# Kernel tuning notes

Measured on AMD Instinct MI355X. Metric: run time of the kernel, lower is better.

## Reference

```python
import jax, jax.numpy as jnp
import numpy as np

G, B, N, D = 3, 4096, 32, 256
C, H, A, L = 128, 8, 128, 16


def setup_inputs() -> dict:
    key = jax.random.key(0)
    ks = jax.random.split(key, 9)
    return {
        "targets": jax.random.normal(ks[0], (B, D), jnp.float32),
        "contexts": jax.random.normal(ks[1], (G, B, N, D), jnp.float32),
        "kernel": jax.random.normal(ks[2], (D, C), jnp.float32) * 0.05,
        "attn_kernel": jax.random.normal(ks[3], (1, H, 2 * C), jnp.float32) * 0.05,
        "attn_bias": jnp.zeros((H * C,), jnp.float32),
        "sem_kernel": jax.random.normal(ks[4], (H * C, A), jnp.float32) * 0.05,
        "sem_att_kernel": jax.random.normal(ks[5], (A, 1), jnp.float32) * 0.05,
        "dense_w": jax.random.normal(ks[6], (H * C, L), jnp.float32) * 0.05,
        "dense_b": jnp.zeros((L,), jnp.float32),
    }


def reference(targets, contexts, kernel, attn_kernel, attn_bias, sem_kernel,
              sem_att_kernel, dense_w, dense_b):
    # NodeAttention (shared weights across metapath groups; vectorized over G)
    node = jnp.einsum('bd,dc->bc', targets, kernel)            # [B,C]
    neigh = jnp.einsum('gbnd,dc->gbnc', contexts, kernel)      # [G,B,N,C]
    g, b, n, c = neigh.shape
    ak = attn_kernel[0]                                        # [H,2C]
    ak_node, ak_neigh = ak[:, :c], ak[:, c:]                   # split of concat([node, neigh])
    # scores[g,b,n,h] = concat(node_b, neigh_gbn) . ak_h
    scores = (jnp.einsum('bc,hc->bh', node, ak_node)[None, :, None, :]
              + jnp.einsum('gbnc,hc->gbnh', neigh, ak_neigh))  # [G,B,N,H]
    scores = jnp.transpose(scores, (0, 1, 3, 2))               # [G,B,H,N]
    coef = jax.nn.softmax(jax.nn.leaky_relu(scores, 0.2), axis=-1)
    z = jnp.einsum('gbhn,gbnc->gbhc', coef, neigh)             # [G,B,H,C]
    z = z.reshape(g, b, -1) + attn_bias                        # [G,B,H*C] (concat=True)
    # SemanticAttention over metapath groups
    inp = jnp.transpose(z, (1, 0, 2))                          # [B,G,HC]
    s = jnp.squeeze(jnp.matmul(jnp.tanh(jnp.matmul(inp, sem_kernel)), sem_att_kernel), -1)  # [B,G]
    att = jax.nn.softmax(s, axis=-1)
    pooled = jnp.einsum('bg,bgd->bd', att, inp)                # [B,HC]
    logits = pooled @ dense_w + dense_b                        # [B,L]
    return logits
```

## Files before the change

### kernel.cpp

```cpp
#include <hip/hip_runtime.h>
#include <hip/hip_bf16.h>

typedef float v4f __attribute__((ext_vector_type(4)));
typedef short v8s __attribute__((ext_vector_type(8)));

__device__ __forceinline__ unsigned short f2bf(float x){
    unsigned u = __float_as_uint(x);
    u += 0x7FFFu + ((u >> 16) & 1u);
    return (unsigned short)(u >> 16);
}
__device__ __forceinline__ float bf2f(unsigned short h){
    return __uint_as_float(((unsigned)h) << 16);
}
__device__ __forceinline__ v8s pack_bf8(v4f a, v4f b){
    union { v8s s; __hip_bfloat162 h[4]; } u;
    u.h[0] = __float22bfloat162_rn(float2{a[0],a[1]});
    u.h[1] = __float22bfloat162_rn(float2{a[2],a[3]});
    u.h[2] = __float22bfloat162_rn(float2{b[0],b[1]});
    u.h[3] = __float22bfloat162_rn(float2{b[2],b[3]});
    return u.s;
}

__global__ __launch_bounds__(256) void prep_all(const float* __restrict__ targ,
        const float* __restrict__ kern, const float* __restrict__ ak,
        const float* __restrict__ semk, float* __restrict__ ns,
        unsigned short* __restrict__ packB, unsigned short* __restrict__ pack2){
    __shared__ float wsh[256*8];
    int blk = blockIdx.x, t = threadIdx.x;
    if (blk < 16){
        {
            float a[8];
            #pragma unroll
            for (int h=0;h<8;h++) a[h]=0.f;
            const float* kr = kern + t*128;
            for (int c=0;c<128;c++){
                float kv = kr[c];
                #pragma unroll
                for (int h=0;h<8;h++) a[h] = fmaf(kv, ak[h*256+c], a[h]);
            }
            #pragma unroll
            for (int h=0;h<8;h++) wsh[t*8+h]=a[h];
        }
        __syncthreads();
        int b = blk*256 + t;
        float acc[8];
        #pragma unroll
        for (int h=0;h<8;h++) acc[h]=0.f;
        const float* tr = targ + (size_t)b*256;
        for (int d=0;d<256;d++){
            float tv = tr[d];
            #pragma unroll
            for (int h=0;h<8;h++) acc[h] = fmaf(tv, wsh[d*8+h], acc[h]);
        }
        #pragma unroll
        for (int h=0;h<8;h++) ns[b*8+h]=acc[h];
    } else if (blk < 18){
        {
            float a[8];
            #pragma unroll
            for (int h=0;h<8;h++) a[h]=0.f;
            const float* kr = kern + t*128;
            for (int c=0;c<128;c++){
                float kv = kr[c];
                #pragma unroll
                for (int h=0;h<8;h++) a[h] = fmaf(kv, ak[h*256+128+c], a[h]);
            }
            #pragma unroll
            for (int h=0;h<8;h++) wsh[t*8+h]=a[h];
        }
        __syncthreads();
        int gt = (blk-16)*256 + t;
        for (int r=0;r<72;r++){
            int e = gt + r*512;
            int j = e & 7; int l = (e>>3) & 63;
            int fc = e >> 9; int cc = fc % 9; int kk = fc / 9;
            int d = kk*32 + (l>>4)*8 + j;
            int c = cc*16 + (l&15);
            float v;
            if (cc < 8) v = kern[d*128 + c];
            else { int h = c - 128; v = (h < 8) ? wsh[d*8+h] : 0.0f; }
            packB[e] = f2bf(v);
        }
    } else {
        int gt = (blk-18)*256 + t;
        for (int r=0;r<16;r++){
            int e = gt + r*8192;
            int j = e & 7; int l = (e>>3) & 63;
            int cc = (e>>9) & 7; int gkk = e >> 12;
            int k = gkk*32 + (l>>4)*8 + j;
            int a2 = cc*16 + (l&15);
            pack2[e] = f2bf(semk[k*128 + a2]);
        }
    }
}

__global__ __launch_bounds__(256,4) void phase1(const float* __restrict__ ctx,
        const unsigned short* __restrict__ packB, const float* __restrict__ ns,
        const float* __restrict__ bias, unsigned short* __restrict__ zb16){
    __shared__ __align__(16) unsigned short outT[4][32*128];
    __shared__ float cf[4][32*8];

    int t = threadIdx.x, w = t >> 6, lane = t & 63;
    int wt = blockIdx.x*4 + w;
    int g = wt >> 12, b = wt & 4095;
    int q = lane >> 4, ct = lane & 15;

    const float* ab = ctx + ((size_t)((g*4096 + b)*32) + ct)*256 + q*8;
    const unsigned short* bbase = packB + lane*8;

    v4f acc0[9], acc1[9];
    #pragma unroll
    for (int i=0;i<9;i++){ acc0[i] = (v4f){0.f,0.f,0.f,0.f}; acc1[i] = (v4f){0.f,0.f,0.f,0.f}; }

    #pragma unroll
    for (int kk=0;kk<8;kk++){
        v8s a0 = pack_bf8(*(const v4f*)(ab + kk*32),        *(const v4f*)(ab + kk*32 + 4));
        v8s a1 = pack_bf8(*(const v4f*)(ab + 4096 + kk*32), *(const v4f*)(ab + 4096 + kk*32 + 4));
        #pragma unroll
        for (int cc=0;cc<9;cc++){
            v8s bf = *(const v8s*)(bbase + (kk*9+cc)*512);
            acc0[cc] = __builtin_amdgcn_mfma_f32_16x16x32_bf16(a0, bf, acc0[cc], 0,0,0);
            acc1[cc] = __builtin_amdgcn_mfma_f32_16x16x32_bf16(a1, bf, acc1[cc], 0,0,0);
        }
    }

    {
        float nsv = (ct < 8) ? ns[b*8 + ct] : 0.f;
        float sc[8];
        #pragma unroll
        for (int r=0;r<4;r++){ sc[r] = acc0[8][r] + nsv; sc[4+r] = acc1[8][r] + nsv; }
        #pragma unroll
        for (int i=0;i<8;i++) sc[i] = sc[i] > 0.f ? sc[i] : 0.2f*sc[i];
        float mx = sc[0];
        #pragma unroll
        for (int i=1;i<8;i++) mx = fmaxf(mx, sc[i]);
        mx = fmaxf(mx, __shfl_xor(mx, 16));
        mx = fmaxf(mx, __shfl_xor(mx, 32));
        float sum = 0.f;
        #pragma unroll
        for (int i=0;i<8;i++){ sc[i] = __expf(sc[i]-mx); sum += sc[i]; }
        sum += __shfl_xor(sum, 16);
        sum += __shfl_xor(sum, 32);
        float inv = 1.0f / sum;
        if (ct < 8){
            #pragma unroll
            for (int r=0;r<4;r++){
                cf[w][(q*4+r)*8 + ct]    = sc[r]*inv;
                cf[w][(16+q*4+r)*8 + ct] = sc[4+r]*inv;
            }
        }
    }

    #pragma unroll
    for (int cc=0;cc<8;cc++){
        #pragma unroll
        for (int r=0;r<4;r++){
            int row0 = q*4+r, row1 = 16+q*4+r;
            int byte0 = (row0*256 + (cc*16+ct)*2) ^ ((row0&7)<<5);
            int byte1 = (row1*256 + (cc*16+ct)*2) ^ ((row1&7)<<5);
            *(unsigned short*)((char*)outT[w] + byte0) = f2bf(acc0[cc][r]);
            *(unsigned short*)((char*)outT[w] + byte1) = f2bf(acc1[cc][r]);
        }
    }

    {
        size_t zb = ((size_t)b*3 + g)*1024;
        int c0i = 2*lane;
        #pragma unroll
        for (int half=0; half<2; ++half){
            float az0[4], az1[4];
            #pragma unroll
            for (int i=0;i<4;i++){ az0[i]=0.f; az1[i]=0.f; }
            for (int n=0;n<32;n++){
                int byte = (n*256 + lane*4) ^ ((n&7)<<5);
                unsigned v = *(const unsigned*)((const char*)outT[w] + byte);
                float v0 = bf2f((unsigned short)(v & 0xffffu));
                float v1 = bf2f((unsigned short)(v >> 16));
                v4f c0 = *(const v4f*)&cf[w][n*8 + half*4];
                az0[0]=fmaf(c0[0],v0,az0[0]); az0[1]=fmaf(c0[1],v0,az0[1]);
                az0[2]=fmaf(c0[2],v0,az0[2]); az0[3]=fmaf(c0[3],v0,az0[3]);
                az1[0]=fmaf(c0[0],v1,az1[0]); az1[1]=fmaf(c0[1],v1,az1[1]);
                az1[2]=fmaf(c0[2],v1,az1[2]); az1[3]=fmaf(c0[3],v1,az1[3]);
            }
            #pragma unroll
            for (int j=0;j<4;j++){
                int hh = half*4 + j;
                unsigned short p0 = f2bf(az0[j] + bias[hh*128 + c0i]);
                unsigned short p1 = f2bf(az1[j] + bias[hh*128 + c0i + 1]);
                unsigned pk = ((unsigned)p1 << 16) | (unsigned)p0;
                *(unsigned*)(zb16 + zb + hh*128 + c0i) = pk;
            }
        }
    }
}

__global__ __launch_bounds__(256) void semk2(const unsigned short* __restrict__ zb16,
        const unsigned short* __restrict__ pack2, const float* __restrict__ sa,
        float* __restrict__ sws){
    __shared__ float red[16*4];
    int t = threadIdx.x, w = t>>6, lane = t&63;
    int r0 = blockIdx.x * 16;
    v4f acc0 = (v4f){0.f,0.f,0.f,0.f};
    v4f acc1 = (v4f){0.f,0.f,0.f,0.f};
    const unsigned short* abase = zb16 + (size_t)(r0 + (lane&15))*1024 + (lane>>4)*8;
    #pragma unroll 4
    for (int kk=0; kk<32; kk++){
        v8s afr = *(const v8s*)(abase + kk*32);
        v8s b0  = *(const v8s*)(pack2 + (((kk*8 + w  )*64 + lane) << 3));
        v8s b1  = *(const v8s*)(pack2 + (((kk*8 + w+4)*64 + lane) << 3));
        acc0 = __builtin_amdgcn_mfma_f32_16x16x32_bf16(afr, b0, acc0, 0,0,0);
        acc1 = __builtin_amdgcn_mfma_f32_16x16x32_bf16(afr, b1, acc1, 0,0,0);
    }
    float sa0 = sa[w*16 + (lane&15)];
    float sa1 = sa[(w+4)*16 + (lane&15)];
    #pragma unroll
    for (int r=0;r<4;r++){
        float v = fmaf(tanhf(acc0[r]), sa0, tanhf(acc1[r]) * sa1);
        #pragma unroll
        for (int d=1; d<16; d<<=1) v += __shfl_xor(v, d);
        if ((lane&15)==0) red[((lane>>4)*4 + r)*4 + w] = v;
    }
    __syncthreads();
    if (t < 16)
        sws[r0 + t] = red[t*4] + red[t*4+1] + red[t*4+2] + red[t*4+3];
}

__global__ __launch_bounds__(64) void final3(const unsigned short* __restrict__ zb16,
        const float* __restrict__ sws, const float* __restrict__ dw,
        const float* __restrict__ db, float* __restrict__ outp){
    int b = blockIdx.x;
    int lane = threadIdx.x;
    float s0 = sws[b*3], s1 = sws[b*3+1], s2 = sws[b*3+2];
    float m = fmaxf(s0, fmaxf(s1, s2));
    float e0 = __expf(s0-m), e1 = __expf(s1-m), e2 = __expf(s2-m);
    float inv = 1.0f/(e0+e1+e2);
    float a0 = e0*inv, a1 = e1*inv, a2 = e2*inv;

    const unsigned short* z0 = zb16 + (size_t)b*3072 + lane*16;
    v8s za0 = *(const v8s*)(z0);          v8s za1 = *(const v8s*)(z0+8);
    v8s zb0 = *(const v8s*)(z0+1024);     v8s zb1 = *(const v8s*)(z0+1032);
    v8s zc0 = *(const v8s*)(z0+2048);     v8s zc1 = *(const v8s*)(z0+2056);
    float p[16];
    #pragma unroll
    for (int k=0;k<8;k++){
        p[k]   = a0*bf2f((unsigned short)za0[k]) + a1*bf2f((unsigned short)zb0[k]) + a2*bf2f((unsigned short)zc0[k]);
        p[k+8] = a0*bf2f((unsigned short)za1[k]) + a1*bf2f((unsigned short)zb1[k]) + a2*bf2f((unsigned short)zc1[k]);
    }
    float acc[16];
    #pragma unroll
    for (int l=0;l<16;l++) acc[l]=0.f;
    #pragma unroll
    for (int k=0;k<16;k++){
        const float* dr = dw + (lane*16 + k)*16;
        v4f d0 = *(const v4f*)(dr);
        v4f d1 = *(const v4f*)(dr+4);
        v4f d2 = *(const v4f*)(dr+8);
        v4f d3 = *(const v4f*)(dr+12);
        float pk = p[k];
        acc[0]=fmaf(pk,d0[0],acc[0]);  acc[1]=fmaf(pk,d0[1],acc[1]);
        acc[2]=fmaf(pk,d0[2],acc[2]);  acc[3]=fmaf(pk,d0[3],acc[3]);
        acc[4]=fmaf(pk,d1[0],acc[4]);  acc[5]=fmaf(pk,d1[1],acc[5]);
        acc[6]=fmaf(pk,d1[2],acc[6]);  acc[7]=fmaf(pk,d1[3],acc[7]);
        acc[8]=fmaf(pk,d2[0],acc[8]);  acc[9]=fmaf(pk,d2[1],acc[9]);
        acc[10]=fmaf(pk,d2[2],acc[10]); acc[11]=fmaf(pk,d2[3],acc[11]);
        acc[12]=fmaf(pk,d3[0],acc[12]); acc[13]=fmaf(pk,d3[1],acc[13]);
        acc[14]=fmaf(pk,d3[2],acc[14]); acc[15]=fmaf(pk,d3[3],acc[15]);
    }
    #pragma unroll
    for (int l=0;l<16;l++){
        float v = acc[l];
        #pragma unroll
        for (int d=1; d<64; d<<=1) v += __shfl_xor(v, d);
        acc[l] = v;
    }
    float myv = 0.f;
    #pragma unroll
    for (int l=0;l<16;l++) myv = (lane==l) ? acc[l] : myv;
    if (lane < 16) outp[b*16 + lane] = myv + db[lane];
}

extern "C" void kernel_launch(void* const* d_in, const int* in_sizes, int n_in,
                              void* d_out, int out_size, void* d_ws, size_t ws_size,
                              hipStream_t stream) {
    const float* targets  = (const float*)d_in[0];
    const float* contexts = (const float*)d_in[1];
    const float* kern     = (const float*)d_in[2];
    const float* ak       = (const float*)d_in[3];
    const float* bias     = (const float*)d_in[4];
    const float* semk     = (const float*)d_in[5];
    const float* sa       = (const float*)d_in[6];
    const float* dw       = (const float*)d_in[7];
    const float* db       = (const float*)d_in[8];
    float* outp = (float*)d_out;

    char* ws = (char*)d_ws;
    unsigned short* packB = (unsigned short*)(ws);
    float* nsb            = (float*)(ws + 73728);
    unsigned short* pack2 = (unsigned short*)(ws + 204800);
    unsigned short* zb16  = (unsigned short*)(ws + 466944);
    float* sws            = (float*)(ws + 25632768);

    prep_all<<<50, 256, 0, stream>>>(targets, kern, ak, semk, nsb, packB, pack2);
    phase1<<<3072, 256, 0, stream>>>(contexts, packB, nsb, bias, zb16);
    semk2<<<768, 256, 0, stream>>>(zb16, pack2, sa, sws);
    final3<<<4096, 64, 0, stream>>>(zb16, sws, dw, db, outp);
}
```

Baseline: 200.4 us.

## Split phase1 into MFMA projection kernel and attention kernel via bf16 scratch

Splits the fused phase1 kernel into two kernels. The first does only the MFMA projection of contexts and writes the bf16 accumulators to a large workspace scratch buffer. The second reads them back and runs the softmax and neighbor aggregation. The fused kernel is kept as a fallback when the workspace is too small. The split is meant to cut register and LDS pressure in the matmul part so more waves can hide memory latency, at the cost of about 113 MB of extra global writes and reads.

Result: slower. 258.9 us (+29.2%).

```diff
diff --git a/kernel.cpp b/kernel.cpp
--- a/kernel.cpp
+++ b/kernel.cpp
@@ -3,6 +3,7 @@
 
 typedef float v4f __attribute__((ext_vector_type(4)));
 typedef short v8s __attribute__((ext_vector_type(8)));
+typedef short v4s __attribute__((ext_vector_type(4)));
 
 __device__ __forceinline__ unsigned short f2bf(float x){
     unsigned u = __float_as_uint(x);
@@ -18,6 +19,12 @@
     u.h[1] = __float22bfloat162_rn(float2{a[2],a[3]});
     u.h[2] = __float22bfloat162_rn(float2{b[0],b[1]});
     u.h[3] = __float22bfloat162_rn(float2{b[2],b[3]});
+    return u.s;
+}
+__device__ __forceinline__ v4s pack_bf4(v4f a){
+    union { v4s s; __hip_bfloat162 h[2]; } u;
+    u.h[0] = __float22bfloat162_rn(float2{a[0],a[1]});
+    u.h[1] = __float22bfloat162_rn(float2{a[2],a[3]});
     return u.s;
 }
 
@@ -94,9 +101,42 @@
     }
 }
 
-__global__ __launch_bounds__(256,4) void phase1(const float* __restrict__ ctx,
-        const unsigned short* __restrict__ packB, const float* __restrict__ ns,
-        const float* __restrict__ bias, unsigned short* __restrict__ zb16){
+__global__ __launch_bounds__(256,4) void p1a(const float* __restrict__ ctx,
+        const unsigned short* __restrict__ packB, unsigned short* __restrict__ scr){
+    int t = threadIdx.x, w = t >> 6, lane = t & 63;
+    int wt = blockIdx.x*4 + w;
+    int q = lane >> 4, ct = lane & 15;
+
+    const float* ab = ctx + (size_t)wt*8192 + ct*256 + q*8;
+    const unsigned short* bbase = packB + lane*8;
+
+    v4f acc0[9], acc1[9];
+    #pragma unroll
+    for (int i=0;i<9;i++){ acc0[i] = (v4f){0.f,0.f,0.f,0.f}; acc1[i] = (v4f){0.f,0.f,0.f,0.f}; }
+
+    #pragma unroll
+    for (int kk=0;kk<8;kk++){
+        v8s a0 = pack_bf8(*(const v4f*)(ab + kk*32),        *(const v4f*)(ab + kk*32 + 4));
+        v8s a1 = pack_bf8(*(const v4f*)(ab + 4096 + kk*32), *(const v4f*)(ab + 4096 + kk*32 + 4));
+        #pragma unroll
+        for (int cc=0;cc<9;cc++){
+            v8s bf = *(const v8s*)(bbase + (kk*9+cc)*512);
+            acc0[cc] = __builtin_amdgcn_mfma_f32_16x16x32_bf16(a0, bf, acc0[cc], 0,0,0);
+            acc1[cc] = __builtin_amdgcn_mfma_f32_16x16x32_bf16(a1, bf, acc1[cc], 0,0,0);
+        }
+    }
+
+    size_t sb = (size_t)wt * 4608;
+    #pragma unroll
+    for (int cc=0;cc<9;cc++){
+        *(v4s*)(scr + sb + (cc*64 + lane)*4)        = pack_bf4(acc0[cc]);
+        *(v4s*)(scr + sb + 2304 + (cc*64 + lane)*4) = pack_bf4(acc1[cc]);
+    }
+}
+
+__global__ __launch_bounds__(256,4) void p1b(const unsigned short* __restrict__ scr,
+        const float* __restrict__ ns, const float* __restrict__ bias,
+        unsigned short* __restrict__ zb16){
     __shared__ __align__(16) unsigned short outT[4][32*128];
     __shared__ float cf[4][32*8];
 
@@ -105,22 +145,16 @@
     int g = wt >> 12, b = wt & 4095;
     int q = lane >> 4, ct = lane & 15;
 
-    const float* ab = ctx + ((size_t)((g*4096 + b)*32) + ct)*256 + q*8;
-    const unsigned short* bbase = packB + lane*8;
-
+    size_t sb = (size_t)wt * 4608;
     v4f acc0[9], acc1[9];
     #pragma unroll
-    for (int i=0;i<9;i++){ acc0[i] = (v4f){0.f,0.f,0.f,0.f}; acc1[i] = (v4f){0.f,0.f,0.f,0.f}; }
-
-    #pragma unroll
-    for (int kk=0;kk<8;kk++){
-        v8s a0 = pack_bf8(*(const v4f*)(ab + kk*32),        *(const v4f*)(ab + kk*32 + 4));
-        v8s a1 = pack_bf8(*(const v4f*)(ab + 4096 + kk*32), *(const v4f*)(ab + 4096 + kk*32 + 4));
-        #pragma unroll
-        for (int cc=0;cc<9;cc++){
-            v8s bf = *(const v8s*)(bbase + (kk*9+cc)*512);
-            acc0[cc] = __builtin_amdgcn_mfma_f32_16x16x32_bf16(a0, bf, acc0[cc], 0,0,0);
-            acc1[cc] = __builtin_amdgcn_mfma_f32_16x16x32_bf16(a1, bf, acc1[cc], 0,0,0);
+    for (int cc=0;cc<9;cc++){
+        v4s x0 = *(const v4s*)(scr + sb + (cc*64 + lane)*4);
+        v4s x1 = *(const v4s*)(scr + sb + 2304 + (cc*64 + lane)*4);
+        #pragma unroll
+        for (int r=0;r<4;r++){
+            acc0[cc][r] = bf2f((unsigned short)x0[r]);
+            acc1[cc][r] = bf2f((unsigned short)x1[r]);
         }
     }
 
@@ -163,6 +197,103 @@
         }
     }
 
+    {
+        size_t zb = ((size_t)b*3 + g)*1024;
+        int c0i = 2*lane;
+        #pragma unroll
+        for (int half=0; half<2; ++half){
+            float az0[4], az1[4];
+            #pragma unroll
+            for (int i=0;i<4;i++){ az0[i]=0.f; az1[i]=0.f; }
+            for (int n=0;n<32;n++){
+                int byte = (n*256 + lane*4) ^ ((n&7)<<5);
+                unsigned v = *(const unsigned*)((const char*)outT[w] + byte);
+                float v0 = bf2f((unsigned short)(v & 0xffffu));
+                float v1 = bf2f((unsigned short)(v >> 16));
+                v4f c0 = *(const v4f*)&cf[w][n*8 + half*4];
+                az0[0]=fmaf(c0[0],v0,az0[0]); az0[1]=fmaf(c0[1],v0,az0[1]);
+                az0[2]=fmaf(c0[2],v0,az0[2]); az0[3]=fmaf(c0[3],v0,az0[3]);
+                az1[0]=fmaf(c0[0],v1,az1[0]); az1[1]=fmaf(c0[1],v1,az1[1]);
+                az1[2]=fmaf(c0[2],v1,az1[2]); az1[3]=fmaf(c0[3],v1,az1[3]);
+            }
+            #pragma unroll
+            for (int j=0;j<4;j++){
+                int hh = half*4 + j;
+                unsigned short p0 = f2bf(az0[j] + bias[hh*128 + c0i]);
+                unsigned short p1 = f2bf(az1[j] + bias[hh*128 + c0i + 1]);
+                unsigned pk = ((unsigned)p1 << 16) | (unsigned)p0;
+                *(unsigned*)(zb16 + zb + hh*128 + c0i) = pk;
+            }
+        }
+    }
+}
+
+__global__ __launch_bounds__(256,4) void phase1_fused(const float* __restrict__ ctx,
+        const unsigned short* __restrict__ packB, const float* __restrict__ ns,
+        const float* __restrict__ bias, unsigned short* __restrict__ zb16){
+    __shared__ __align__(16) unsigned short outT[4][32*128];
+    __shared__ float cf[4][32*8];
+
+    int t = threadIdx.x, w = t >> 6, lane = t & 63;
+    int wt = blockIdx.x*4 + w;
+    int g = wt >> 12, b = wt & 4095;
+    int q = lane >> 4, ct = lane & 15;
+
+    const float* ab = ctx + (size_t)wt*8192 + ct*256 + q*8;
+    const unsigned short* bbase = packB + lane*8;
+
+    v4f acc0[9], acc1[9];
+    #pragma unroll
+    for (int i=0;i<9;i++){ acc0[i] = (v4f){0.f,0.f,0.f,0.f}; acc1[i] = (v4f){0.f,0.f,0.f,0.f}; }
+
+    #pragma unroll
+    for (int kk=0;kk<8;kk++){
+        v8s a0 = pack_bf8(*(const v4f*)(ab + kk*32),        *(const v4f*)(ab + kk*32 + 4));
+        v8s a1 = pack_bf8(*(const v4f*)(ab + 4096 + kk*32), *(const v4f*)(ab + 4096 + kk*32 + 4));
+        #pragma unroll
+        for (int cc=0;cc<9;cc++){
+            v8s bf = *(const v8s*)(bbase + (kk*9+cc)*512);
+            acc0[cc] = __builtin_amdgcn_mfma_f32_16x16x32_bf16(a0, bf, acc0[cc], 0,0,0);
+            acc1[cc] = __builtin_amdgcn_mfma_f32_16x16x32_bf16(a1, bf, acc1[cc], 0,0,0);
+        }
+    }
+    {
+        float nsv = (ct < 8) ? ns[b*8 + ct] : 0.f;
+        float sc[8];
+        #pragma unroll
+        for (int r=0;r<4;r++){ sc[r] = acc0[8][r] + nsv; sc[4+r] = acc1[8][r] + nsv; }
+        #pragma unroll
+        for (int i=0;i<8;i++) sc[i] = sc[i] > 0.f ? sc[i] : 0.2f*sc[i];
+        float mx = sc[0];
+        #pragma unroll
+        for (int i=1;i<8;i++) mx = fmaxf(mx, sc[i]);
+        mx = fmaxf(mx, __shfl_xor(mx, 16));
+        mx = fmaxf(mx, __shfl_xor(mx, 32));
+        float sum = 0.f;
+        #pragma unroll
+        for (int i=0;i<8;i++){ sc[i] = __expf(sc[i]-mx); sum += sc[i]; }
+        sum += __shfl_xor(sum, 16);
+        sum += __shfl_xor(sum, 32);
+        float inv = 1.0f / sum;
+        if (ct < 8){
+            #pragma unroll
+            for (int r=0;r<4;r++){
+                cf[w][(q*4+r)*8 + ct]    = sc[r]*inv;
+                cf[w][(16+q*4+r)*8 + ct] = sc[4+r]*inv;
+            }
+        }
+    }
+    #pragma unroll
+    for (int cc=0;cc<8;cc++){
+        #pragma unroll
+        for (int r=0;r<4;r++){
+            int row0 = q*4+r, row1 = 16+q*4+r;
+            int byte0 = (row0*256 + (cc*16+ct)*2) ^ ((row0&7)<<5);
+            int byte1 = (row1*256 + (cc*16+ct)*2) ^ ((row1&7)<<5);
+            *(unsigned short*)((char*)outT[w] + byte0) = f2bf(acc0[cc][r]);
+            *(unsigned short*)((char*)outT[w] + byte1) = f2bf(acc1[cc][r]);
+        }
+    }
     {
         size_t zb = ((size_t)b*3 + g)*1024;
         int c0i = 2*lane;
@@ -299,9 +430,16 @@
     unsigned short* pack2 = (unsigned short*)(ws + 204800);
     unsigned short* zb16  = (unsigned short*)(ws + 466944);
     float* sws            = (float*)(ws + 25632768);
+    unsigned short* scr   = (unsigned short*)(ws + 25690112);
+    const size_t need = 25690112ULL + 113246208ULL;
 
     prep_all<<<50, 256, 0, stream>>>(targets, kern, ak, semk, nsb, packB, pack2);
-    phase1<<<3072, 256, 0, stream>>>(contexts, packB, nsb, bias, zb16);
+    if (ws_size >= need){
+        p1a<<<3072, 256, 0, stream>>>(contexts, packB, scr);
+        p1b<<<3072, 256, 0, stream>>>(scr, nsb, bias, zb16);
+    } else {
+        phase1_fused<<<3072, 256, 0, stream>>>(contexts, packB, nsb, bias, zb16);
+    }
     semk2<<<768, 256, 0, stream>>>(zb16, pack2, sa, sws);
     final3<<<4096, 64, 0, stream>>>(zb16, sws, dw, db, outp);
 }
```

## Make phase1 persistent with LDS-staged weights and register double-buffered context loads

Applied to the files above, without the earlier changes.

phase1 now launches 256 persistent blocks, one per CU, and each wave walks 12 (g,b) tiles instead of one. The packed weight matrix is copied once per block into shared memory, so it is no longer re-read from global memory per tile. Context data for the next tile is prefetched into registers in two halves while MFMAs run on the current tile. The cost is one block per CU with few waves to hide latency, and heavy register pressure from the 32 v4f prefetch buffers plus the accumulators.

New measurement: 410.2 us. +104.7%, slower.

```diff
diff --git a/kernel.cpp b/kernel.cpp
--- a/kernel.cpp
+++ b/kernel.cpp
@@ -94,101 +94,136 @@
     }
 }
 
-__global__ __launch_bounds__(256,4) void phase1(const float* __restrict__ ctx,
+#define P1_LOADH(BUF, TL, HF) {                                               \
+    const float* ab_ = ctx + (size_t)(TL)*8192 + (HF)*128 + ct*256 + q*8;     \
+    _Pragma("unroll")                                                         \
+    for (int k_=0;k_<4;k_++){                                                 \
+        BUF[4*k_+0] = *(const v4f*)(ab_ + k_*32);                             \
+        BUF[4*k_+1] = *(const v4f*)(ab_ + k_*32 + 4);                         \
+        BUF[4*k_+2] = *(const v4f*)(ab_ + 4096 + k_*32);                      \
+        BUF[4*k_+3] = *(const v4f*)(ab_ + 4096 + k_*32 + 4);                  \
+    } }
+
+#define P1_MFMAH(BUF, HF) {                                                   \
+    _Pragma("unroll")                                                         \
+    for (int k_=0;k_<4;k_++){                                                 \
+        v8s a0_ = pack_bf8(BUF[4*k_+0], BUF[4*k_+1]);                         \
+        v8s a1_ = pack_bf8(BUF[4*k_+2], BUF[4*k_+3]);                         \
+        _Pragma("unroll")                                                     \
+        for (int cc_=0;cc_<9;cc_++){                                          \
+            v8s bf_ = *(const v8s*)(bbase + ((((HF)*4+k_)*9+cc_) << 9));      \
+            acc0[cc_] = __builtin_amdgcn_mfma_f32_16x16x32_bf16(a0_, bf_, acc0[cc_], 0,0,0); \
+            acc1[cc_] = __builtin_amdgcn_mfma_f32_16x16x32_bf16(a1_, bf_, acc1[cc_], 0,0,0); \
+        }                                                                     \
+    } }
+
+__global__ __launch_bounds__(256,1) void phase1(const float* __restrict__ ctx,
         const unsigned short* __restrict__ packB, const float* __restrict__ ns,
         const float* __restrict__ bias, unsigned short* __restrict__ zb16){
+    __shared__ __align__(16) unsigned short bl[36864];
     __shared__ __align__(16) unsigned short outT[4][32*128];
     __shared__ float cf[4][32*8];
 
     int t = threadIdx.x, w = t >> 6, lane = t & 63;
-    int wt = blockIdx.x*4 + w;
-    int g = wt >> 12, b = wt & 4095;
     int q = lane >> 4, ct = lane & 15;
 
-    const float* ab = ctx + ((size_t)((g*4096 + b)*32) + ct)*256 + q*8;
-    const unsigned short* bbase = packB + lane*8;
-
-    v4f acc0[9], acc1[9];
-    #pragma unroll
-    for (int i=0;i<9;i++){ acc0[i] = (v4f){0.f,0.f,0.f,0.f}; acc1[i] = (v4f){0.f,0.f,0.f,0.f}; }
-
-    #pragma unroll
-    for (int kk=0;kk<8;kk++){
-        v8s a0 = pack_bf8(*(const v4f*)(ab + kk*32),        *(const v4f*)(ab + kk*32 + 4));
-        v8s a1 = pack_bf8(*(const v4f*)(ab + 4096 + kk*32), *(const v4f*)(ab + 4096 + kk*32 + 4));
-        #pragma unroll
-        for (int cc=0;cc<9;cc++){
-            v8s bf = *(const v8s*)(bbase + (kk*9+cc)*512);
-            acc0[cc] = __builtin_amdgcn_mfma_f32_16x16x32_bf16(a0, bf, acc0[cc], 0,0,0);
-            acc1[cc] = __builtin_amdgcn_mfma_f32_16x16x32_bf16(a1, bf, acc1[cc], 0,0,0);
-        }
-    }
-
     {
-        float nsv = (ct < 8) ? ns[b*8 + ct] : 0.f;
-        float sc[8];
-        #pragma unroll
-        for (int r=0;r<4;r++){ sc[r] = acc0[8][r] + nsv; sc[4+r] = acc1[8][r] + nsv; }
-        #pragma unroll
-        for (int i=0;i<8;i++) sc[i] = sc[i] > 0.f ? sc[i] : 0.2f*sc[i];
-        float mx = sc[0];
-        #pragma unroll
-        for (int i=1;i<8;i++) mx = fmaxf(mx, sc[i]);
-        mx = fmaxf(mx, __shfl_xor(mx, 16));
-        mx = fmaxf(mx, __shfl_xor(mx, 32));
-        float sum = 0.f;
-        #pragma unroll
-        for (int i=0;i<8;i++){ sc[i] = __expf(sc[i]-mx); sum += sc[i]; }
-        sum += __shfl_xor(sum, 16);
-        sum += __shfl_xor(sum, 32);
-        float inv = 1.0f / sum;
-        if (ct < 8){
+        const v8s* src = (const v8s*)packB;
+        v8s* dst = (v8s*)bl;
+        #pragma unroll
+        for (int r=0;r<18;r++) dst[t + r*256] = src[t + r*256];
+    }
+    __syncthreads();
+
+    const unsigned short* bbase = bl + lane*8;
+    int wid = blockIdx.x*4 + w;
+    int tbase = wid*12;
+
+    v4f Ab0[16], Ab1[16];
+    P1_LOADH(Ab0, tbase, 0);
+    P1_LOADH(Ab1, tbase, 1);
+
+    #pragma unroll 1
+    for (int tt=0; tt<12; ++tt){
+        int tl = tbase + tt;
+        int g = tl >> 12, b = tl & 4095;
+        int nx = (tt < 11) ? tl + 1 : tl;
+
+        v4f acc0[9], acc1[9];
+        #pragma unroll
+        for (int i=0;i<9;i++){ acc0[i] = (v4f){0.f,0.f,0.f,0.f}; acc1[i] = (v4f){0.f,0.f,0.f,0.f}; }
+
+        P1_MFMAH(Ab0, 0);
+        P1_LOADH(Ab0, nx, 0);
+        P1_MFMAH(Ab1, 1);
+        P1_LOADH(Ab1, nx, 1);
+
+        {
+            float nsv = (ct < 8) ? ns[b*8 + ct] : 0.f;
+            float sc[8];
+            #pragma unroll
+            for (int r=0;r<4;r++){ sc[r] = acc0[8][r] + nsv; sc[4+r] = acc1[8][r] + nsv; }
+            #pragma unroll
+            for (int i=0;i<8;i++) sc[i] = sc[i] > 0.f ? sc[i] : 0.2f*sc[i];
+            float mx = sc[0];
+            #pragma unroll
+            for (int i=1;i<8;i++) mx = fmaxf(mx, sc[i]);
+            mx = fmaxf(mx, __shfl_xor(mx, 16));
+            mx = fmaxf(mx, __shfl_xor(mx, 32));
+            float sum = 0.f;
+            #pragma unroll
+            for (int i=0;i<8;i++){ sc[i] = __expf(sc[i]-mx); sum += sc[i]; }
+            sum += __shfl_xor(sum, 16);
+            sum += __shfl_xor(sum, 32);
+            float inv = 1.0f / sum;
+            if (ct < 8){
+                #pragma unroll
+                for (int r=0;r<4;r++){
+                    cf[w][(q*4+r)*8 + ct]    = sc[r]*inv;
+                    cf[w][(16+q*4+r)*8 + ct] = sc[4+r]*inv;
+                }
+            }
+        }
+
+        #pragma unroll
+        for (int cc=0;cc<8;cc++){
             #pragma unroll
             for (int r=0;r<4;r++){
-                cf[w][(q*4+r)*8 + ct]    = sc[r]*inv;
-                cf[w][(16+q*4+r)*8 + ct] = sc[4+r]*inv;
-            }
-        }
-    }
-
-    #pragma unroll
-    for (int cc=0;cc<8;cc++){
-        #pragma unroll
-        for (int r=0;r<4;r++){
-            int row0 = q*4+r, row1 = 16+q*4+r;
-            int byte0 = (row0*256 + (cc*16+ct)*2) ^ ((row0&7)<<5);
-            int byte1 = (row1*256 + (cc*16+ct)*2) ^ ((row1&7)<<5);
-            *(unsigned short*)((char*)outT[w] + byte0) = f2bf(acc0[cc][r]);
-            *(unsigned short*)((char*)outT[w] + byte1) = f2bf(acc1[cc][r]);
-        }
-    }
-
-    {
-        size_t zb = ((size_t)b*3 + g)*1024;
-        int c0i = 2*lane;
-        #pragma unroll
-        for (int half=0; half<2; ++half){
-            float az0[4], az1[4];
-            #pragma unroll
-            for (int i=0;i<4;i++){ az0[i]=0.f; az1[i]=0.f; }
-            for (int n=0;n<32;n++){
-                int byte = (n*256 + lane*4) ^ ((n&7)<<5);
-                unsigned v = *(const unsigned*)((const char*)outT[w] + byte);
-                float v0 = bf2f((unsigned short)(v & 0xffffu));
-                float v1 = bf2f((unsigned short)(v >> 16));
-                v4f c0 = *(const v4f*)&cf[w][n*8 + half*4];
-                az0[0]=fmaf(c0[0],v0,az0[0]); az0[1]=fmaf(c0[1],v0,az0[1]);
-                az0[2]=fmaf(c0[2],v0,az0[2]); az0[3]=fmaf(c0[3],v0,az0[3]);
-                az1[0]=fmaf(c0[0],v1,az1[0]); az1[1]=fmaf(c0[1],v1,az1[1]);
-                az1[2]=fmaf(c0[2],v1,az1[2]); az1[3]=fmaf(c0[3],v1,az1[3]);
-            }
-            #pragma unroll
-            for (int j=0;j<4;j++){
-                int hh = half*4 + j;
-                unsigned short p0 = f2bf(az0[j] + bias[hh*128 + c0i]);
-                unsigned short p1 = f2bf(az1[j] + bias[hh*128 + c0i + 1]);
-                unsigned pk = ((unsigned)p1 << 16) | (unsigned)p0;
-                *(unsigned*)(zb16 + zb + hh*128 + c0i) = pk;
+                int row0 = q*4+r, row1 = 16+q*4+r;
+                int byte0 = (row0*256 + (cc*16+ct)*2) ^ ((row0&7)<<5);
+                int byte1 = (row1*256 + (cc*16+ct)*2) ^ ((row1&7)<<5);
+                *(unsigned short*)((char*)outT[w] + byte0) = f2bf(acc0[cc][r]);
+                *(unsigned short*)((char*)outT[w] + byte1) = f2bf(acc1[cc][r]);
+            }
+        }
+
+        {
+            size_t zb = ((size_t)b*3 + g)*1024;
+            int c0i = 2*lane;
+            #pragma unroll
+            for (int half=0; half<2; ++half){
+                float az0[4], az1[4];
+                #pragma unroll
+                for (int i=0;i<4;i++){ az0[i]=0.f; az1[i]=0.f; }
+                for (int n=0;n<32;n++){
+                    int byte = (n*256 + lane*4) ^ ((n&7)<<5);
+                    unsigned v = *(const unsigned*)((const char*)outT[w] + byte);
+                    float v0 = bf2f((unsigned short)(v & 0xffffu));
+                    float v1 = bf2f((unsigned short)(v >> 16));
+                    v4f c0 = *(const v4f*)&cf[w][n*8 + half*4];
+                    az0[0]=fmaf(c0[0],v0,az0[0]); az0[1]=fmaf(c0[1],v0,az0[1]);
+                    az0[2]=fmaf(c0[2],v0,az0[2]); az0[3]=fmaf(c0[3],v0,az0[3]);
+                    az1[0]=fmaf(c0[0],v1,az1[0]); az1[1]=fmaf(c0[1],v1,az1[1]);
+                    az1[2]=fmaf(c0[2],v1,az1[2]); az1[3]=fmaf(c0[3],v1,az1[3]);
+                }
+                #pragma unroll
+                for (int j=0;j<4;j++){
+                    int hh = half*4 + j;
+                    unsigned short p0 = f2bf(az0[j] + bias[hh*128 + c0i]);
+                    unsigned short p1 = f2bf(az1[j] + bias[hh*128 + c0i + 1]);
+                    unsigned pk = ((unsigned)p1 << 16) | (unsigned)p0;
+                    *(unsigned*)(zb16 + zb + hh*128 + c0i) = pk;
+                }
             }
         }
     }
@@ -301,7 +336,7 @@
     float* sws            = (float*)(ws + 25632768);
 
     prep_all<<<50, 256, 0, stream>>>(targets, kern, ak, semk, nsb, packB, pack2);
-    phase1<<<3072, 256, 0, stream>>>(contexts, packB, nsb, bias, zb16);
+    phase1<<<256, 256, 0, stream>>>(contexts, packB, nsb, bias, zb16);
     semk2<<<768, 256, 0, stream>>>(zb16, pack2, sa, sws);
     final3<<<4096, 64, 0, stream>>>(zb16, sws, dw, db, outp);
 }
```
